# Kernel optimization log

Measured on AMD Instinct MI355X. Metric: run time of the kernel, lower is better.

## Reference

```python
import jax, jax.numpy as jnp
import numpy as np

K = 24  # patch size (SiFinder.KERNEL_SIZE)


def _x_patches(x_dec):
    # non-overlapping KxK patches in raster order (rows of patches, then cols)
    C, H, W = x_dec.shape[1], x_dec.shape[2], x_dec.shape[3]
    p = x_dec[0].reshape(C, H // K, K, W // K, K)
    p = p.transpose(1, 3, 0, 2, 4).reshape(-1, C, K, K)  # (P, C, K, K)
    return p


def _conv(inp, w):
    return jax.lax.conv_general_dilated(
        inp, w, window_strides=(1, 1), padding='VALID',
        dimension_numbers=('NCHW', 'OIHW', 'NCHW'))


def _pearson_corr(x_patches, y):
    # x_patches: (P,C,K,K), y: (1,C,H,W) -> corr map (1,P,H-K+1,W-K+1)
    C = y.shape[1]
    n = K * K  # patch_size per channel-row as in the torch code (K*K)
    mean_x = jnp.mean(x_patches, axis=(1, 2, 3))[None, :, None, None]
    sum_x2 = jnp.sum(x_patches ** 2, axis=(1, 2, 3))[None, :, None, None]
    ones = jnp.ones((1, C, K, K), y.dtype)
    sum_y = _conv(y, ones)          # (1,1,Hc,Wc), broadcast over P
    sum_y2 = _conv(y ** 2, ones)    # (1,1,Hc,Wc)
    sum_xy = _conv(y, x_patches)    # (1,P,Hc,Wc)
    numerator = sum_xy - mean_x * sum_y
    den_x = jnp.sqrt(sum_x2 - n * mean_x * mean_x)
    den_y = jnp.sqrt(sum_y2 - sum_y * sum_y / n)
    return numerator / (den_x * den_y)


def reference(x_dec, y_dec, y):
    xp = _x_patches(x_dec)                 # (P,C,K,K)
    corr = _pearson_corr(xp, y_dec)        # (1,P,Hc,Wc)
    P, Hc, Wc = corr.shape[1], corr.shape[2], corr.shape[3]
    idx = jnp.argmax(corr.reshape(P, Hc * Wc), axis=-1)
    row = idx // Wc
    col = idx % Wc
    # roi_align with boxes [-0.5+col, -0.5+row, -0.5+col+K, -0.5+row+K],
    # output K, spatial_scale=1, sampling_ratio=-1, aligned=False reduces to
    # exact integer-offset patch extraction y[0,:,row:row+K, col:col+K].
    yc = y[0]
    C = yc.shape[0]
    def gather(r, c):
        return jax.lax.dynamic_slice(yc, (0, r, c), (C, K, K))
    y_patches = jax.vmap(gather)(row, col)  # (P,C,K,K)
    return y_patches


def setup_inputs() -> dict:
    key = jax.random.key(0)
    k1, k2, k3 = jax.random.split(key, 3)
    x_dec = jax.random.normal(k1, (1, 3, 384, 384), dtype=jnp.float32)
    y_dec = jax.random.normal(k2, (1, 3, 768, 768), dtype=jnp.float32)
    y = jax.random.normal(k3, (1, 3, 768, 768), dtype=jnp.float32)
    return {"x_dec": x_dec, "y_dec": y_dec, "y": y}
```

## Files before the change

kernel.cpp:

```cpp
#include <hip/hip_runtime.h>

typedef float v16f __attribute__((ext_vector_type(16)));
typedef int v8i __attribute__((ext_vector_type(8)));
typedef int v4i __attribute__((ext_vector_type(4)));
typedef int v2i __attribute__((ext_vector_type(2)));
typedef unsigned short ushort_t;
typedef unsigned char uchar_t;
typedef long long ll_t;

#define HH 768
#define WW 768
#define CH 3
#define KS 24
#define HC 745
#define WC 745
#define NP 256
#define XH 384
#define XW 384

#define NBX 24
#define NBY 187
#define NBLK (NBX*NBY)
#define BROWS 4
#define BCOLS 32
#define NSTEP 27
#define NCAND 8
#define NGRID (8*1152)

__device__ __forceinline__ ushort_t f2bf(float f) {
    union { __bf16 h; ushort_t u; } cv; cv.h = (__bf16)f; return cv.u;
}
__device__ __forceinline__ float bf2f(ushort_t u) {
    union { unsigned u; float f; } cv; cv.u = ((unsigned)u) << 16; return cv.f;
}
__device__ __forceinline__ uchar_t f2e4m3(float f) {
    unsigned u = __float_as_uint(f);
    unsigned s = (u >> 24) & 0x80;
    float a = fabsf(f);
    if (a < 0.0078125f) {
        int q = (int)(a * 512.0f + 0.5f);
        return (uchar_t)(s | (unsigned)q);
    }
    int e = (int)((u >> 23) & 0xFF);
    unsigned m = (u >> 20) & 7;
    unsigned rest = u & 0xFFFFF;
    if (rest > 0x80000 || (rest == 0x80000 && (m & 1))) { m++; if (m == 8) { m = 0; e++; } }
    int e8 = e - 120;
    if (e8 <= 0) { int q = (int)(a * 512.0f + 0.5f); if (q > 7) q = 7; return (uchar_t)(s | q); }
    if (e8 > 15) return (uchar_t)(s | 0x7E);
    return (uchar_t)(s | ((unsigned)e8 << 3) | m);
}


__global__ void k_colsum(const float* __restrict__ y, float* __restrict__ ksum,
                         float* __restrict__ ksum2) {
    int idx = blockIdx.x * 256 + threadIdx.x;
    if (idx >= HH * WW) return;
    float a = y[idx], b = y[idx + HH * WW], c = y[idx + 2 * HH * WW];
    ksum[idx]  = a + b + c;
    ksum2[idx] = a * a + b * b + c * c;
}

__global__ void k_hsum(const float* __restrict__ ksum, const float* __restrict__ ksum2,
                       float* __restrict__ h1, float* __restrict__ h2) {
    int idx = blockIdx.x * 256 + threadIdx.x;
    if (idx >= HH * WC) return;
    int h = idx / WC, w = idx % WC;
    const float* r  = ksum  + h * WW + w;
    const float* r2 = ksum2 + h * WW + w;
    float s = 0.f, s2 = 0.f;
    #pragma unroll
    for (int j = 0; j < KS; j++) { s += r[j]; s2 += r2[j]; }
    h1[idx] = s; h2[idx] = s2;
}

__global__ void k_vsum(const float* __restrict__ h1, const float* __restrict__ h2,
                       unsigned* __restrict__ sv) {
    int idx = blockIdx.x * 256 + threadIdx.x;
    if (idx >= HC * WC) return;
    int r = idx / WC, w = idx % WC;
    float s = 0.f, s2 = 0.f;
    #pragma unroll
    for (int i = 0; i < KS; i++) { s += h1[(r + i) * WC + w]; s2 += h2[(r + i) * WC + w]; }
    float d2 = s2 - s * s * (1.0f / 576.0f);
    sv[idx] = ((unsigned)f2bf(rsqrtf(fmaxf(d2, 1e-20f))) << 16) | (unsigned)f2bf(s);
}

__global__ void k_meanx(const float* __restrict__ x, float* __restrict__ mx) {
    int p = blockIdx.x;
    int pr = p >> 4, pc = p & 15;
    float s = 0.f;
    for (int e = threadIdx.x; e < CH * KS * KS; e += 256) {
        int c = e / (KS * KS); int rem = e % (KS * KS);
        int i = rem / KS, j = rem % KS;
        s += x[(c * XH + pr * KS + i) * XW + pc * KS + j];
    }
    __shared__ float red[256];
    red[threadIdx.x] = s; __syncthreads();
    for (int st = 128; st > 0; st >>= 1) {
        if (threadIdx.x < st) red[threadIdx.x] += red[threadIdx.x + st];
        __syncthreads();
    }
    if (threadIdx.x == 0) mx[p] = red[0] * (1.0f / 1728.0f);
}

__global__ void k_bmat8(const float* __restrict__ x, uchar_t* __restrict__ bmk) {
    int p = blockIdx.x; int pr = p >> 4, pc = p & 15;
    for (int e = threadIdx.x; e < CH * KS * KS; e += 256) {
        int c = e / (KS * KS), rem = e % (KS * KS), i = rem / KS, j = rem % KS;
        int o = (j >> 3) * 72 + c * 24 + i;
        int s = o >> 3, w = o & 7;
        int hh = w >> 2, q = w & 3;
        bmk[(((size_t)(s * 2 + hh) * 2 + (q >> 1)) * 256 + p) * 16 + (q & 1) * 8 + (j & 7)] =
            f2e4m3(x[(c * XH + pr * KS + i) * XW + pc * KS + j]);
    }
}

__global__ void k_y4(const float* __restrict__ yd, uchar_t* __restrict__ y4) {
    int idx = blockIdx.x * 256 + threadIdx.x;
    if (idx >= 4 * 3 * HH * (WW / 4)) return;
    int q = idx % (WW / 4); int rem = idx / (WW / 4);
    int r = rem % HH; rem /= HH;
    int c = rem % 3; int S = rem / 3;
    const float* src = yd + (c * HH + r) * WW;
    union { uchar_t u[4]; unsigned v; } o;
    #pragma unroll
    for (int qq = 0; qq < 4; qq++) {
        int t = q * 4 + qq + S;
        o.u[qq] = f2e4m3(t < WW ? src[t] : 0.f);
    }
    ((unsigned*)(y4 + ((size_t)(S * 3 + c) * HH + r) * WW))[q] = o.v;
}


#define KBODY(ADc, BFc, ADn, DOB)                                             \
  do {                                                                        \
    {                                                                         \
      const uchar_t* Ap = Abase0 + U;                                         \
      _Pragma("unroll")                                                       \
      for (int r = 0; r < 7; r++) {                                           \
        ADn[r].x = *(const int*)(Ap + r * 56);                                \
        ADn[r].y = *(const int*)(Ap + r * 56 + 4);                            \
      }                                                                       \
      if (++j3 < 3) U += 448;                                                 \
      else { j3 = 0; if (++c3 < 3) U += 672; else { c3 = 0; U -= 4024; } }    \
    }                                                                         \
    _Pragma("unroll")                                                         \
    for (int mt = 0; mt < 4; mt++) {                                          \
      v8i af8;                                                                \
      _Pragma("unroll")                                                       \
      for (int q = 0; q < 4; q++) {                                           \
        af8[2 * q] = ADc[mt + q].x; af8[2 * q + 1] = ADc[mt + q].y;           \
      }                                                                       \
      acc[mt] = __builtin_amdgcn_mfma_scale_f32_32x32x64_f8f6f4(              \
          af8, BFc, acc[mt], 0, 0, 0, 0x7F7F7F7F, 0, 0x7F7F7F7F);             \
    }                                                                         \
    if (DOB) {                                                                \
      v4i b0 = *(const v4i*)(gBbase + gBoff);                                 \
      v4i b1 = *(const v4i*)(gBbase + gBoff + 4096);                          \
      BFc = __builtin_shufflevector(b0, b1, 0, 1, 2, 3, 4, 5, 6, 7);          \
      gBoff += 16384;                                                         \
    }                                                                         \
  } while (0)

__global__ __launch_bounds__(256, 3) void k_corr(
    const uchar_t* __restrict__ y4, const uchar_t* __restrict__ bmk,
    const unsigned* __restrict__ sv, const float* __restrict__ mx,
    ushort_t* __restrict__ ps16)
{
    const int xcd = blockIdx.x & 7;
    const int idx = blockIdx.x >> 3;
    const int bstart = (NBY * xcd) >> 3;
    const int bcnt = ((NBY * (xcd + 1)) >> 3) - bstart;
    const int local_by = idx / 48;
    if (local_by >= bcnt) return;
    const int rem = idx - local_by * 48;
    const int z = rem / 24;
    const int bx = rem - z * 24;
    const int by = bstart + local_by;

    __shared__ __align__(16) uchar_t Aband[19072];

    const int tid = threadIdx.x;
    const int wave = tid >> 6, lane = tid & 63;
    const int r0 = by * BROWS, w0 = bx * BCOLS;
    const int zbase = z * 128;
    const int l31 = lane & 31, h = lane >> 5;
    const int wn = wave;

    const uchar_t* gBbase = bmk + h * 8192 + (size_t)(zbase + wn * 32 + l31) * 16;

    v8i bfA, bfB;
    {
        v4i b0 = *(const v4i*)(gBbase);
        v4i b1 = *(const v4i*)(gBbase + 4096);
        bfA = __builtin_shufflevector(b0, b1, 0, 1, 2, 3, 4, 5, 6, 7);
        v4i b2 = *(const v4i*)(gBbase + 16384);
        v4i b3 = *(const v4i*)(gBbase + 16384 + 4096);
        bfB = __builtin_shufflevector(b2, b3, 0, 1, 2, 3, 4, 5, 6, 7);
    }

    for (int e = tid; e < 4704; e += 256) {
        int dw = e % 14;
        int row84 = (e / 14) % 84;
        int S = e / 1176;
        int c = row84 / 28, r = row84 - c * 28;
        int gr = r0 + r; gr = gr < HH ? gr : HH - 1;
        unsigned v = *(const unsigned*)(y4 + ((size_t)(S * 3 + c) * HH + gr) * WW + w0 + dw * 4);
        *(unsigned*)(Aband + S * 4768 + row84 * 56 + dw * 4) = v;
    }

    const uchar_t* Abase0 = Aband + (l31 & 3) * 4767 + l31 + h * 224;

    v16f acc[4];
    #pragma unroll
    for (int a = 0; a < 4; a++)
        #pragma unroll
        for (int r = 0; r < 16; r++) acc[a][r] = 0.f;

    __syncthreads();

    v2i adA[7], adB[7];
    #pragma unroll
    for (int r = 0; r < 7; r++) {
        adA[r].x = *(const int*)(Abase0 + r * 56);
        adA[r].y = *(const int*)(Abase0 + r * 56 + 4);
    }
    int U = 448, j3 = 1, c3 = 0;
    int gBoff = 2 * 16384;

    #pragma unroll 1
    for (int p = 0; p < 12; p++) {
        KBODY(adA, bfA, adB, 1);
        KBODY(adB, bfB, adA, 1);
    }
    KBODY(adA, bfA, adB, 1);
    KBODY(adB, bfB, adA, 0);
    {
        #pragma unroll
        for (int mt = 0; mt < 4; mt++) {
            v8i af8;
            #pragma unroll
            for (int q = 0; q < 4; q++) {
                af8[2 * q] = adA[mt + q].x; af8[2 * q + 1] = adA[mt + q].y;
            }
            acc[mt] = __builtin_amdgcn_mfma_scale_f32_32x32x64_f8f6f4(
                af8, bfA, acc[mt], 0, 0, 0, 0x7F7F7F7F, 0, 0x7F7F7F7F);
        }
    }

    float mxp = mx[zbase + wn * 32 + l31];
    float best = -1e30f;
    #pragma unroll
    for (int mt = 0; mt < 4; mt++) {
        int rg = r0 + mt;
        #pragma unroll
        for (int r = 0; r < 16; r++) {
            int row32 = (r & 3) + 8 * (r >> 2) + 4 * h;
            int wg = w0 + row32;
            bool valid = (rg < HC) && (wg < WC);
            int pos = rg * WC + wg;
            unsigned pv = valid ? sv[pos] : 0u;
            float S1 = bf2f((ushort_t)(pv & 0xFFFF));
            float iv = bf2f((ushort_t)(pv >> 16));
            float sc = valid ? (acc[mt][r] - mxp * S1) * iv : -1e30f;
            best = fmaxf(best, sc);
        }
    }
    best = fmaxf(best, __shfl_xor(best, 32));
    if (h == 0)
        ps16[(by * NBX + bx) * NP + zbase + wn * 32 + l31] = f2bf(best);
}


__global__ void k_select(const ushort_t* __restrict__ ps16, int* __restrict__ cand) {
    int p = blockIdx.x, tid = threadIdx.x;
    __shared__ float ls[NBLK];
    __shared__ float rs[256];
    __shared__ int   ri[256];
    for (int e = tid; e < NBLK; e += 256) ls[e] = bf2f(ps16[e * NP + p]);
    __syncthreads();
    for (int round = 0; round < NCAND; round++) {
        float bs = -1e38f; int bi = 0;
        for (int e = tid; e < NBLK; e += 256) if (ls[e] > bs) { bs = ls[e]; bi = e; }
        rs[tid] = bs; ri[tid] = bi; __syncthreads();
        for (int st = 128; st > 0; st >>= 1) {
            if (tid < st && rs[tid + st] > rs[tid]) { rs[tid] = rs[tid + st]; ri[tid] = ri[tid + st]; }
            __syncthreads();
        }
        int win = ri[0];
        if (tid == 0) cand[p * NCAND + round] = win;
        if (tid == (win & 255)) ls[win] = -1e38f;
        __syncthreads();
    }
}


__global__ void k_rescore(const int* __restrict__ cand, const float* __restrict__ xdec,
                          const float* __restrict__ ydec, const float* __restrict__ mx,
                          const float* __restrict__ yfull, float* __restrict__ out) {
    int p = blockIdx.x, tid = threadIdx.x;
    int pr = p >> 4, pc = p & 15;
    float mxp = mx[p];
    float best = -1e30f; int bpos = 0x7FFFFFFF;
    #pragma unroll 1
    for (int cdp = 0; cdp < 4; cdp++) {
        int cd = cdp * 2 + (tid >> 7);
        int blk = cand[p * NCAND + cd];
        int r0 = (blk / NBX) * BROWS, w0 = (blk % NBX) * BCOLS;
        int pi = tid & 127;
        int rg = r0 + (pi >> 5), wg = w0 + (pi & 31);
        if (rg < HC && wg < WC) {
            float sxy = 0.f, sy = 0.f, sy2 = 0.f;
            for (int c = 0; c < CH; c++) {
                #pragma unroll 1
                for (int i = 0; i < KS; i++) {
                    const float* yr = ydec + (c * HH + rg + i) * WW + wg;
                    const float* xr = xdec + (c * XH + pr * KS + i) * XW + pc * KS;
                    #pragma unroll
                    for (int j = 0; j < KS; j++) {
                        float yv = yr[j];
                        sxy = fmaf(yv, xr[j], sxy);
                        sy += yv;
                        sy2 = fmaf(yv, yv, sy2);
                    }
                }
            }
            float d2 = sy2 - sy * sy * (1.0f / 576.0f);
            int pos = rg * WC + wg;
            float sc = (sxy - mxp * sy) * rsqrtf(fmaxf(d2, 1e-20f));
            if (sc > best || (sc == best && pos < bpos)) { best = sc; bpos = pos; }
        }
    }
    __shared__ float rs[256];
    __shared__ int   ri[256];
    rs[tid] = best; ri[tid] = bpos; __syncthreads();
    for (int st = 128; st > 0; st >>= 1) {
        if (tid < st) {
            if (rs[tid + st] > rs[tid] || (rs[tid + st] == rs[tid] && ri[tid + st] < ri[tid])) {
                rs[tid] = rs[tid + st]; ri[tid] = ri[tid + st];
            }
        }
        __syncthreads();
    }
    int bestpos = ri[0];
    int row = bestpos / WC, col = bestpos % WC;
    for (int e = tid; e < CH * KS * KS; e += 256) {
        int c = e / (KS * KS), rem = e % (KS * KS), i = rem / KS, j = rem % KS;
        out[p * CH * KS * KS + e] = yfull[(c * HH + row + i) * WW + col + j];
    }
}


extern "C" void kernel_launch(void* const* d_in, const int* in_sizes, int n_in,
                              void* d_out, int out_size, void* d_ws, size_t ws_size,
                              hipStream_t stream) {
    const float* xdec = (const float*)d_in[0];
    const float* ydec = (const float*)d_in[1];
    const float* y    = (const float*)d_in[2];
    float* out = (float*)d_out;

    float* ws = (float*)d_ws;
    unsigned* sv    = (unsigned*)(ws + 0);
    float*    mx    = ws + 555040;
    uchar_t*  Bmk   = (uchar_t*)(ws + 555296);
    int*      cand  = (int*)(ws + 665888);
    ushort_t* ps16  = (ushort_t*)(ws + 667936);
    uchar_t*  y4    = (uchar_t*)(ws + 1242400);
    float* ksum  = ws + 667936;
    float* ksum2 = ws + 1257760;
    float* h1    = ws + 1847584;
    float* h2    = ws + 2419744;

    k_colsum<<<(HH * WW + 255) / 256, 256, 0, stream>>>(ydec, ksum, ksum2);
    k_hsum<<<(HH * WC + 255) / 256, 256, 0, stream>>>(ksum, ksum2, h1, h2);
    k_vsum<<<(HC * WC + 255) / 256, 256, 0, stream>>>(h1, h2, sv);
    k_meanx<<<NP, 256, 0, stream>>>(xdec, mx);
    k_bmat8<<<NP, 256, 0, stream>>>(xdec, Bmk);
    k_y4<<<(4 * 3 * HH * (WW / 4) + 255) / 256, 256, 0, stream>>>(ydec, y4);

    k_corr<<<NGRID, 256, 0, stream>>>(y4, Bmk, sv, mx, ps16);
    k_select<<<NP, 256, 0, stream>>>(ps16, cand);
    k_rescore<<<NP, 256, 0, stream>>>(cand, xdec, ydec, mx, y, out);
}
```

Baseline: 484.8 us.

## Fuse box-sum and mean kernels, split rescore across candidates for parallelism

```diff
diff --git a/kernel.cpp b/kernel.cpp
--- a/kernel.cpp
+++ b/kernel.cpp
@@ -52,26 +52,24 @@
 }
 
 
-__global__ void k_colsum(const float* __restrict__ y, float* __restrict__ ksum,
-                         float* __restrict__ ksum2) {
-    int idx = blockIdx.x * 256 + threadIdx.x;
-    if (idx >= HH * WW) return;
-    float a = y[idx], b = y[idx + HH * WW], c = y[idx + 2 * HH * WW];
-    ksum[idx]  = a + b + c;
-    ksum2[idx] = a * a + b * b + c * c;
-}
-
-__global__ void k_hsum(const float* __restrict__ ksum, const float* __restrict__ ksum2,
-                       float* __restrict__ h1, float* __restrict__ h2) {
-    int idx = blockIdx.x * 256 + threadIdx.x;
-    if (idx >= HH * WC) return;
-    int h = idx / WC, w = idx % WC;
-    const float* r  = ksum  + h * WW + w;
-    const float* r2 = ksum2 + h * WW + w;
-    float s = 0.f, s2 = 0.f;
-    #pragma unroll
-    for (int j = 0; j < KS; j++) { s += r[j]; s2 += r2[j]; }
-    h1[idx] = s; h2[idx] = s2;
+__global__ void k_rowsum(const float* __restrict__ y, float* __restrict__ h1,
+                         float* __restrict__ h2) {
+    int r = blockIdx.x;
+    __shared__ float ks[WW], ks2[WW];
+    for (int t = threadIdx.x; t < WW; t += 256) {
+        float a = y[(0 * HH + r) * WW + t];
+        float b = y[(1 * HH + r) * WW + t];
+        float c = y[(2 * HH + r) * WW + t];
+        ks[t]  = a + b + c;
+        ks2[t] = a * a + b * b + c * c;
+    }
+    __syncthreads();
+    for (int w = threadIdx.x; w < WC; w += 256) {
+        float s = 0.f, s2 = 0.f;
+        #pragma unroll
+        for (int j = 0; j < KS; j++) { s += ks[w + j]; s2 += ks2[w + j]; }
+        h1[r * WC + w] = s; h2[r * WC + w] = s2;
+    }
 }
 
 __global__ void k_vsum(const float* __restrict__ h1, const float* __restrict__ h2,
@@ -86,34 +84,27 @@
     sv[idx] = ((unsigned)f2bf(rsqrtf(fmaxf(d2, 1e-20f))) << 16) | (unsigned)f2bf(s);
 }
 
-__global__ void k_meanx(const float* __restrict__ x, float* __restrict__ mx) {
-    int p = blockIdx.x;
-    int pr = p >> 4, pc = p & 15;
-    float s = 0.f;
-    for (int e = threadIdx.x; e < CH * KS * KS; e += 256) {
-        int c = e / (KS * KS); int rem = e % (KS * KS);
-        int i = rem / KS, j = rem % KS;
-        s += x[(c * XH + pr * KS + i) * XW + pc * KS + j];
-    }
-    __shared__ float red[256];
-    red[threadIdx.x] = s; __syncthreads();
-    for (int st = 128; st > 0; st >>= 1) {
-        if (threadIdx.x < st) red[threadIdx.x] += red[threadIdx.x + st];
-        __syncthreads();
-    }
-    if (threadIdx.x == 0) mx[p] = red[0] * (1.0f / 1728.0f);
-}
-
-__global__ void k_bmat8(const float* __restrict__ x, uchar_t* __restrict__ bmk) {
+__global__ void k_bmat8(const float* __restrict__ x, uchar_t* __restrict__ bmk,
+                        float* __restrict__ mx) {
     int p = blockIdx.x; int pr = p >> 4, pc = p & 15;
+    float sum = 0.f;
     for (int e = threadIdx.x; e < CH * KS * KS; e += 256) {
         int c = e / (KS * KS), rem = e % (KS * KS), i = rem / KS, j = rem % KS;
+        float v = x[(c * XH + pr * KS + i) * XW + pc * KS + j];
+        sum += v;
         int o = (j >> 3) * 72 + c * 24 + i;
         int s = o >> 3, w = o & 7;
         int hh = w >> 2, q = w & 3;
         bmk[(((size_t)(s * 2 + hh) * 2 + (q >> 1)) * 256 + p) * 16 + (q & 1) * 8 + (j & 7)] =
-            f2e4m3(x[(c * XH + pr * KS + i) * XW + pc * KS + j]);
-    }
+            f2e4m3(v);
+    }
+    __shared__ float red[256];
+    red[threadIdx.x] = sum; __syncthreads();
+    for (int st = 128; st > 0; st >>= 1) {
+        if (threadIdx.x < st) red[threadIdx.x] += red[threadIdx.x + st];
+        __syncthreads();
+    }
+    if (threadIdx.x == 0) mx[p] = red[0] * (1.0f / 1728.0f);
 }
 
 __global__ void k_y4(const float* __restrict__ yd, uchar_t* __restrict__ y4) {
@@ -296,46 +287,42 @@
 }
 
 
-__global__ void k_rescore(const int* __restrict__ cand, const float* __restrict__ xdec,
-                          const float* __restrict__ ydec, const float* __restrict__ mx,
-                          const float* __restrict__ yfull, float* __restrict__ out) {
-    int p = blockIdx.x, tid = threadIdx.x;
+__global__ void k_rescore2(const int* __restrict__ cand, const float* __restrict__ xdec,
+                           const float* __restrict__ ydec, const float* __restrict__ mx,
+                           float* __restrict__ rsc, int* __restrict__ rpo) {
+    int bid = blockIdx.x;
+    int p = bid >> 3, cd = bid & 7;
+    int tid = threadIdx.x;
     int pr = p >> 4, pc = p & 15;
-    float mxp = mx[p];
+    int blk = cand[p * NCAND + cd];
+    int r0 = (blk / NBX) * BROWS, w0 = (blk % NBX) * BCOLS;
+    int rg = r0 + (tid >> 5), wg = w0 + (tid & 31);
     float best = -1e30f; int bpos = 0x7FFFFFFF;
-    #pragma unroll 1
-    for (int cdp = 0; cdp < 4; cdp++) {
-        int cd = cdp * 2 + (tid >> 7);
-        int blk = cand[p * NCAND + cd];
-        int r0 = (blk / NBX) * BROWS, w0 = (blk % NBX) * BCOLS;
-        int pi = tid & 127;
-        int rg = r0 + (pi >> 5), wg = w0 + (pi & 31);
-        if (rg < HC && wg < WC) {
-            float sxy = 0.f, sy = 0.f, sy2 = 0.f;
-            for (int c = 0; c < CH; c++) {
-                #pragma unroll 1
-                for (int i = 0; i < KS; i++) {
-                    const float* yr = ydec + (c * HH + rg + i) * WW + wg;
-                    const float* xr = xdec + (c * XH + pr * KS + i) * XW + pc * KS;
-                    #pragma unroll
-                    for (int j = 0; j < KS; j++) {
-                        float yv = yr[j];
-                        sxy = fmaf(yv, xr[j], sxy);
-                        sy += yv;
-                        sy2 = fmaf(yv, yv, sy2);
-                    }
+    if (rg < HC && wg < WC) {
+        float mxp = mx[p];
+        float sxy = 0.f, sy = 0.f, sy2 = 0.f;
+        for (int c = 0; c < CH; c++) {
+            #pragma unroll 1
+            for (int i = 0; i < KS; i++) {
+                const float* yr = ydec + (c * HH + rg + i) * WW + wg;
+                const float* xr = xdec + (c * XH + pr * KS + i) * XW + pc * KS;
+                #pragma unroll
+                for (int j = 0; j < KS; j++) {
+                    float yv = yr[j];
+                    sxy = fmaf(yv, xr[j], sxy);
+                    sy += yv;
+                    sy2 = fmaf(yv, yv, sy2);
                 }
             }
-            float d2 = sy2 - sy * sy * (1.0f / 576.0f);
-            int pos = rg * WC + wg;
-            float sc = (sxy - mxp * sy) * rsqrtf(fmaxf(d2, 1e-20f));
-            if (sc > best || (sc == best && pos < bpos)) { best = sc; bpos = pos; }
-        }
-    }
-    __shared__ float rs[256];
-    __shared__ int   ri[256];
+        }
+        float d2 = sy2 - sy * sy * (1.0f / 576.0f);
+        best = (sxy - mxp * sy) * rsqrtf(fmaxf(d2, 1e-20f));
+        bpos = rg * WC + wg;
+    }
+    __shared__ float rs[128];
+    __shared__ int   ri[128];
     rs[tid] = best; ri[tid] = bpos; __syncthreads();
-    for (int st = 128; st > 0; st >>= 1) {
+    for (int st = 64; st > 0; st >>= 1) {
         if (tid < st) {
             if (rs[tid + st] > rs[tid] || (rs[tid + st] == rs[tid] && ri[tid + st] < ri[tid])) {
                 rs[tid] = rs[tid + st]; ri[tid] = ri[tid + st];
@@ -343,8 +330,25 @@
         }
         __syncthreads();
     }
-    int bestpos = ri[0];
-    int row = bestpos / WC, col = bestpos % WC;
+    if (tid == 0) { rsc[bid] = rs[0]; rpo[bid] = ri[0]; }
+}
+
+
+__global__ void k_final(const float* __restrict__ rsc, const int* __restrict__ rpo,
+                        const float* __restrict__ yfull, float* __restrict__ out) {
+    int p = blockIdx.x, tid = threadIdx.x;
+    __shared__ int bp;
+    if (tid == 0) {
+        float best = -1e30f; int bpos = 0x7FFFFFFF;
+        for (int cd = 0; cd < NCAND; cd++) {
+            float s = rsc[p * NCAND + cd];
+            int   q = rpo[p * NCAND + cd];
+            if (s > best || (s == best && q < bpos)) { best = s; bpos = q; }
+        }
+        bp = bpos;
+    }
+    __syncthreads();
+    int row = bp / WC, col = bp % WC;
     for (int e = tid; e < CH * KS * KS; e += 256) {
         int c = e / (KS * KS), rem = e % (KS * KS), i = rem / KS, j = rem % KS;
         out[p * CH * KS * KS + e] = yfull[(c * HH + row + i) * WW + col + j];
@@ -367,19 +371,18 @@
     int*      cand  = (int*)(ws + 665888);
     ushort_t* ps16  = (ushort_t*)(ws + 667936);
     uchar_t*  y4    = (uchar_t*)(ws + 1242400);
-    float* ksum  = ws + 667936;
-    float* ksum2 = ws + 1257760;
+    float*    rsc   = ws + 3011872;
+    int*      rpo   = (int*)(ws + 3013920);
     float* h1    = ws + 1847584;
     float* h2    = ws + 2419744;
 
-    k_colsum<<<(HH * WW + 255) / 256, 256, 0, stream>>>(ydec, ksum, ksum2);
-    k_hsum<<<(HH * WC + 255) / 256, 256, 0, stream>>>(ksum, ksum2, h1, h2);
+    k_rowsum<<<HH, 256, 0, stream>>>(ydec, h1, h2);
     k_vsum<<<(HC * WC + 255) / 256, 256, 0, stream>>>(h1, h2, sv);
-    k_meanx<<<NP, 256, 0, stream>>>(xdec, mx);
-    k_bmat8<<<NP, 256, 0, stream>>>(xdec, Bmk);
+    k_bmat8<<<NP, 256, 0, stream>>>(xdec, Bmk, mx);
     k_y4<<<(4 * 3 * HH * (WW / 4) + 255) / 256, 256, 0, stream>>>(ydec, y4);
 
     k_corr<<<NGRID, 256, 0, stream>>>(y4, Bmk, sv, mx, ps16);
     k_select<<<NP, 256, 0, stream>>>(ps16, cand);
-    k_rescore<<<NP, 256, 0, stream>>>(cand, xdec, ydec, mx, y, out);
-}
+    k_rescore2<<<NP * NCAND, 128, 0, stream>>>(cand, xdec, ydec, mx, rsc, rpo);
+    k_final<<<NP, 256, 0, stream>>>(rsc, rpo, y, out);
+}
```

After: 421.4 us. 1.15x faster.
